# Optimization experiments

Measured on AMD Instinct MI355X. Metric: run time of the kernel, lower is better.

Reference implementation:

```python
import jax, jax.numpy as jnp
import numpy as np

D_MODEL = 512
NUM_HEADS = 8
HEAD_DIM = D_MODEL // NUM_HEADS
SEQ_LEN = 4096
BATCH = 2
D_FF = 4 * D_MODEL
EPS = 1e-5


def _layer_norm(x, g, b):
    mu = jnp.mean(x, axis=-1, keepdims=True)
    var = jnp.var(x, axis=-1, keepdims=True)
    return (x - mu) * jax.lax.rsqrt(var + EPS) * g + b


def setup_inputs() -> dict:
    key = jax.random.key(0)
    ks = jax.random.split(key, 12)
    s = 0.02
    inp = {
        "x": jax.random.normal(ks[0], (BATCH, SEQ_LEN, D_MODEL), jnp.float32),
        # Linear weights stored as [in, out] (y = x @ W + b)
        "Wq": jax.random.normal(ks[1], (D_MODEL, D_MODEL), jnp.float32) * s,
        "bq": jnp.zeros((D_MODEL,), jnp.float32),
        "Wk": jax.random.normal(ks[2], (D_MODEL, D_MODEL), jnp.float32) * s,
        "bk": jnp.zeros((D_MODEL,), jnp.float32),
        "Wv": jax.random.normal(ks[3], (D_MODEL, D_MODEL), jnp.float32) * s,
        "bv": jnp.zeros((D_MODEL,), jnp.float32),
        "Wo": jax.random.normal(ks[4], (D_MODEL, D_MODEL), jnp.float32) * s,
        "bo": jnp.zeros((D_MODEL,), jnp.float32),
        "ln1_g": jnp.ones((D_MODEL,), jnp.float32),
        "ln1_b": jnp.zeros((D_MODEL,), jnp.float32),
        "ln2_g": jnp.ones((D_MODEL,), jnp.float32),
        "ln2_b": jnp.zeros((D_MODEL,), jnp.float32),
        "W1": jax.random.normal(ks[5], (D_MODEL, D_FF), jnp.float32) * s,
        "b1": jnp.zeros((D_FF,), jnp.float32),
        "W2": jax.random.normal(ks[6], (D_FF, D_MODEL), jnp.float32) * s,
        "b2": jnp.zeros((D_MODEL,), jnp.float32),
    }
    return inp


def reference(x, Wq, bq, Wk, bk, Wv, bv, Wo, bo, ln1_g, ln1_b, ln2_g, ln2_b, W1, b1, W2, b2):
    B, S, D = x.shape
    residual = x
    h = _layer_norm(x, ln1_g, ln1_b)
    # project and split heads: [B, H, S, Dh]
    def split_heads(t):
        return t.reshape(B, S, NUM_HEADS, HEAD_DIM).transpose(0, 2, 1, 3)
    q = split_heads(h @ Wq + bq)
    k = split_heads(h @ Wk + bk)
    v = split_heads(h @ Wv + bv)
    scores = jnp.einsum("bhqd,bhkd->bhqk", q, k) / (HEAD_DIM ** 0.5)
    attn = jax.nn.softmax(scores, axis=-1)
    out = jnp.einsum("bhqk,bhkd->bhqd", attn, v)
    out = out.transpose(0, 2, 1, 3).reshape(B, S, D)
    out = out @ Wo + bo
    x1 = residual + out
    h2 = _layer_norm(x1, ln2_g, ln2_b)
    ff = jax.nn.gelu(h2 @ W1 + b1, approximate=False) @ W2 + b2
    return x1 + ff
```

## Files before the change

kernel.cpp:

```cpp
#include <hip/hip_runtime.h>
#include <hip/hip_bf16.h>
#include <math.h>

typedef __hip_bfloat16 bf16;

#define D_MODEL 512
#define NUM_HEADS 8
#define HEAD_DIM 64
#define SEQ_LEN 4096
#define BATCH 2
#define D_FF 2048
#define TOKENS (BATCH * SEQ_LEN)
#define QKV_STRIDE 1536
#define KSPLIT 2

typedef short short4v __attribute__((ext_vector_type(4)));
typedef short short8v __attribute__((ext_vector_type(8)));
typedef float float4v __attribute__((ext_vector_type(4)));
typedef float float2v __attribute__((ext_vector_type(2)));

union frag_u { short8v v8; short4v v4[2]; short s[8]; };
union pack_u { unsigned u[2]; short4v v4; };

__device__ __forceinline__ float b2f(bf16 v) { return __bfloat162float(v); }
__device__ __forceinline__ bf16 f2b(float v) { return __float2bfloat16(v); }
__device__ __forceinline__ short f2bs(float v) { bf16 t = __float2bfloat16(v); return *(short*)&t; }
__device__ __forceinline__ float exp2fast(float x) { return __builtin_amdgcn_exp2f(x); }

__device__ __forceinline__ unsigned pack_bf16(float lo, float hi) {
    unsigned a = __float_as_uint(hi) + 0x8000u;
    unsigned b = __float_as_uint(lo) + 0x8000u;
    return __builtin_amdgcn_perm(a, b, 0x07060302u);
}

__device__ __forceinline__ unsigned cvt_pk_bf16(float lo, float hi) {
    unsigned r;
    asm("v_cvt_pk_bf16_f32 %0, %1, %2" : "=v"(r) : "v"(lo), "v"(hi));
    return r;
}

__device__ __forceinline__ int3 swz_xyz() {
    int gx = gridDim.x, gy = gridDim.y;
    int id = blockIdx.x + gx * (blockIdx.y + gy * blockIdx.z);
    int nwg = gx * gy * (int)gridDim.z;
    int nid = (id & 7) * (nwg >> 3) + (id >> 3);
    int3 r;
    r.x = nid % gx;
    int t = nid / gx;
    r.y = t % gy;
    r.z = t / gy;
    return r;
}

#define AS1(p) ((__attribute__((address_space(1))) void*)(p))
#define AS3(p) ((__attribute__((address_space(3))) void*)(p))

__device__ __forceinline__ int self_detect(const unsigned* __restrict__ xw, int tid) {
    unsigned w = xw[tid & 63];
    unsigned e = (w >> 7) & 0xFFu;
    unsigned long long b = __ballot(e >= 110 && e <= 140);
    return __popcll(b) < 32;
}

__device__ __forceinline__ void do_tr(const void* __restrict__ src, bf16* __restrict__ dst,
                                      int K, int N, int n0, int k0, int fl, int tid,
                                      bf16 (*tile)[65]) {
    int c = tid & 63, r4 = tid >> 6;
#pragma unroll
    for (int t = 0; t < 16; t++) {
        int r = t * 4 + r4;
        size_t si = (size_t)(k0 + r) * N + n0 + c;
        float v = fl ? ((const float*)src)[si] : b2f(((const bf16*)src)[si]);
        tile[r][c] = f2b(v);
    }
    __syncthreads();
#pragma unroll
    for (int t = 0; t < 16; t++) {
        int r = t * 4 + r4;
        dst[(size_t)(n0 + r) * K + k0 + c] = tile[c][r];
    }
}

__global__ void prep_ln_kernel(const void* x, const void* Wq, const void* Wk, const void* Wv,
                               const void* Wo, const void* W1, const void* W2,
                               const void* bq, const void* bk, const void* bv, const void* bo,
                               const void* b1, const void* b2,
                               const void* g1, const void* e1, const void* g2, const void* e2,
                               bf16* __restrict__ Wqkvt ,
                               bf16* __restrict__ W1t, bf16* __restrict__ W2t,
                               bf16* __restrict__ small, int* __restrict__ flag,
                               bf16* __restrict__ hb) {
    __shared__ bf16 tile[64][65];
    __shared__ float rs[4], rss[4], stat[2];
    int blk = blockIdx.x, tid = threadIdx.x;
    int fl = self_detect((const unsigned*)x, tid);
    if (blk == 0 && tid == 0) flag[0] = fl;
    if (blk < 256) {
        int z = blk >> 6, tt = blk & 63;
        const void* src = (z == 0) ? Wq : (z == 1) ? Wk : (z == 2) ? Wv : Wo;
        do_tr(src, Wqkvt + (size_t)z * 512 * 512, 512, 512, (tt & 7) * 64, (tt >> 3) * 64,
              fl, tid, tile);
    } else if (blk < 512) {
        int tt = blk - 256;
        do_tr(W1, W1t, 512, 2048, (tt & 31) * 64, (tt >> 5) * 64, fl, tid, tile);
    } else if (blk < 768) {
        int tt = blk - 512;
        do_tr(W2, W2t, 2048, 512, (tt & 7) * 64, (tt >> 3) * 64, fl, tid, tile);
    } else if (blk < 794) {
        int i = (blk - 768) * 256 + tid;
        const void* src; int off;
        if (i < 512)       { src = bq; off = 0; }
        else if (i < 1024) { src = bk; off = 512; }
        else if (i < 1536) { src = bv; off = 1024; }
        else if (i < 2048) { src = bo; off = 1536; }
        else if (i < 4096) { src = b1; off = 2048; }
        else if (i < 4608) { src = b2; off = 4096; }
        else if (i < 5120) { src = g1; off = 4608; }
        else if (i < 5632) { src = e1; off = 5120; }
        else if (i < 6144) { src = g2; off = 5632; }
        else               { src = e2; off = 6144; }
        int j = i - off;
        small[i] = fl ? f2b(((const float*)src)[j]) : ((const bf16*)src)[j];
    } else {
        int t = blk - 794;
        float v0, v1, gg0, gg1, bb0, bb1;
        if (fl) {
            const float* xr = (const float*)x + (size_t)t * D_MODEL;
            v0 = xr[tid]; v1 = xr[tid + 256];
            gg0 = ((const float*)g1)[tid]; gg1 = ((const float*)g1)[tid + 256];
            bb0 = ((const float*)e1)[tid]; bb1 = ((const float*)e1)[tid + 256];
        } else {
            const bf16* xr = (const bf16*)x + (size_t)t * D_MODEL;
            v0 = b2f(xr[tid]); v1 = b2f(xr[tid + 256]);
            gg0 = b2f(((const bf16*)g1)[tid]); gg1 = b2f(((const bf16*)g1)[tid + 256]);
            bb0 = b2f(((const bf16*)e1)[tid]); bb1 = b2f(((const bf16*)e1)[tid + 256]);
        }
        float s = v0 + v1, ss = v0 * v0 + v1 * v1;
        for (int o = 32; o > 0; o >>= 1) {
            s += __shfl_down(s, o);
            ss += __shfl_down(ss, o);
        }
        int w = tid >> 6, l = tid & 63;
        if (l == 0) { rs[w] = s; rss[w] = ss; }
        __syncthreads();
        if (tid == 0) {
            float S = rs[0] + rs[1] + rs[2] + rs[3];
            float SS = rss[0] + rss[1] + rss[2] + rss[3];
            float mu = S / (float)D_MODEL;
            float var = SS / (float)D_MODEL - mu * mu;
            stat[0] = mu;
            stat[1] = rsqrtf(var + 1e-5f);
        }
        __syncthreads();
        float mu = stat[0], rstd = stat[1];
        bf16* orow = hb + (size_t)t * D_MODEL;
        orow[tid]       = f2b((v0 - mu) * rstd * gg0 + bb0);
        orow[tid + 256] = f2b((v1 - mu) * rstd * gg1 + bb1);
    }
}

template <int MODE>
__global__ void ln_kernel(const void* __restrict__ xv, const bf16* __restrict__ g,
                          const bf16* __restrict__ b, bf16* __restrict__ out,
                          const int* __restrict__ flag) {
    int t = blockIdx.x;
    int tid = threadIdx.x;
    int fl = (MODE == 2) ? *flag : 0;
    float v0, v1;
    if (fl) {
        const float* xr = (const float*)xv + (size_t)t * D_MODEL;
        v0 = xr[tid]; v1 = xr[tid + 256];
    } else {
        const bf16* xr = (const bf16*)xv + (size_t)t * D_MODEL;
        v0 = b2f(xr[tid]); v1 = b2f(xr[tid + 256]);
    }
    float s = v0 + v1, ss = v0 * v0 + v1 * v1;
    for (int o = 32; o > 0; o >>= 1) {
        s += __shfl_down(s, o);
        ss += __shfl_down(ss, o);
    }
    __shared__ float rs[4], rss[4], stat[2];
    int w = tid >> 6, l = tid & 63;
    if (l == 0) { rs[w] = s; rss[w] = ss; }
    __syncthreads();
    if (tid == 0) {
        float S = rs[0] + rs[1] + rs[2] + rs[3];
        float SS = rss[0] + rss[1] + rss[2] + rss[3];
        float mu = S / (float)D_MODEL;
        float var = SS / (float)D_MODEL - mu * mu;
        stat[0] = mu;
        stat[1] = rsqrtf(var + 1e-5f);
    }
    __syncthreads();
    float mu = stat[0], rstd = stat[1];
    bf16* orow = out + (size_t)t * D_MODEL;
    orow[tid]       = f2b((v0 - mu) * rstd * b2f(g[tid])       + b2f(b[tid]));
    orow[tid + 256] = f2b((v1 - mu) * rstd * b2f(g[tid + 256]) + b2f(b[tid + 256]));
}

__device__ __forceinline__ float gelu_tanh(float v) {
    float u = 0.7978845608f * (v + 0.044715f * v * v * v);
    float e2 = __expf(-2.f * u);
    return v / (1.f + e2);
}

template <int ACT, int RES, int OUTMODE, int VT>
__global__ __launch_bounds__(256) void mfma_gemm64(
    const bf16* __restrict__ A, const bf16* __restrict__ Wt,
    const bf16* __restrict__ bias, const void* __restrict__ res,
    void* __restrict__ Cout, bf16* __restrict__ Vt_out,
    const int* __restrict__ flag, int M, int N, int K) {
    __shared__ bf16 As[2][128 * 32];
    __shared__ bf16 Bs[2][64 * 32];
    int tid = threadIdx.x, wave = tid >> 6, lane = tid & 63;
    int m = lane & 15, g = lane >> 4;
    int3 sw = swz_xyz();
    int row0 = sw.y * 128, col0 = sw.x * 64;
    int R0 = wave * 32;
    int fl = (OUTMODE == 2 || RES == 3) ? *flag : 0;
    float4v acc[2][4] = {};

    int srow = lane >> 2;
    int scol = (lane & 3) * 8;
    const bf16* Ab = A  + (size_t)(row0 + wave * 32 + srow) * K + scol;
    const bf16* Bb = Wt + (size_t)(col0 + wave * 16 + srow) * K + scol;

#define GSTAGE64(buf, kk0)                                                         \
    {                                                                              \
        _Pragma("unroll")                                                          \
        for (int t = 0; t < 2; t++)                                                \
            __builtin_amdgcn_global_load_lds(AS1(Ab + (size_t)(t * 16) * K + (kk0)),\
                AS3(&As[buf][(wave * 32 + t * 16) * 32]), 16, 0, 0);               \
        __builtin_amdgcn_global_load_lds(AS1(Bb + (kk0)),                          \
            AS3(&Bs[buf][(wave * 16) * 32]), 16, 0, 0);                            \
    }

    int nk = K >> 5;
    GSTAGE64(0, 0);
    __syncthreads();
    for (int it = 0; it < nk; it++) {
        int cur = it & 1;
        if (it + 1 < nk) GSTAGE64(cur ^ 1, (it + 1) * 32);
        short8v fa[2], fb[4];
#pragma unroll
        for (int i = 0; i < 2; i++)
            fa[i] = *(const short8v*)&As[cur][(R0 + i * 16 + m) * 32 + g * 8];
#pragma unroll
        for (int j = 0; j < 4; j++)
            fb[j] = *(const short8v*)&Bs[cur][(j * 16 + m) * 32 + g * 8];
        __builtin_amdgcn_s_setprio(1);
#pragma unroll
        for (int i = 0; i < 2; i++)
#pragma unroll
            for (int j = 0; j < 4; j++)
                acc[i][j] = __builtin_amdgcn_mfma_f32_16x16x32_bf16(fa[i], fb[j], acc[i][j], 0, 0, 0);
        __builtin_amdgcn_s_setprio(0);
        __syncthreads();
    }
#undef GSTAGE64

    if (VT && col0 >= 1024) {
#pragma unroll
        for (int i = 0; i < 2; i++) {
            int row = row0 + R0 + i * 16 + g * 4;
            int b = row >> 12, s = row & (SEQ_LEN - 1);
#pragma unroll
            for (int j = 0; j < 4; j++) {
                int col = col0 + j * 16 + m;
                int hh = (col - 1024) >> 6, d = col & 63;
                float bi = b2f(bias[col]);
                pack_u oo;
                oo.u[0] = pack_bf16(acc[i][j][0] + bi, acc[i][j][1] + bi);
                oo.u[1] = pack_bf16(acc[i][j][2] + bi, acc[i][j][3] + bi);
                *(short4v*)&Vt_out[((size_t)((b << 3) + hh) * 64 + d) * SEQ_LEN + s] = oo.v4;
            }
        }
        return;
    }

#pragma unroll
    for (int i = 0; i < 2; i++) {
#pragma unroll
        for (int r = 0; r < 4; r++) {
            int row = row0 + R0 + i * 16 + g * 4 + r;
#pragma unroll
            for (int j = 0; j < 4; j++) {
                int col = col0 + j * 16 + m;
                float v = acc[i][j][r] + b2f(bias[col]);
                if (ACT == 1) v = gelu_tanh(v);
                size_t idx = (size_t)row * N + col;
                if (RES == 2) v += b2f(((const bf16*)res)[idx]);
                if (RES == 3) v += fl ? ((const float*)res)[idx]
                                      : b2f(((const bf16*)res)[idx]);
                if (OUTMODE == 0) ((bf16*)Cout)[idx] = f2b(v);
                else {
                    if (fl) ((float*)Cout)[idx] = v;
                    else ((bf16*)Cout)[idx] = f2b(v);
                }
            }
        }
    }
}

#define F3(a, b, c) fmaxf(fmaxf((a), (b)), (c))
template <int KS>
__global__ __launch_bounds__(256, 4) void flash_attn(const bf16* __restrict__ Q,
                                                     const bf16* __restrict__ K,
                                                     const bf16* __restrict__ Vt_g,
                                                     bf16* __restrict__ Op,
                                                     float2* __restrict__ mlout) {
    __shared__ bf16 Ks[64][72];
    __shared__ bf16 Vt[64][72];

    int tid = threadIdx.x;
    int wave = tid >> 6, lane = tid & 63;
    int m = lane & 15, g = lane >> 4;
    bf16* PtW = &Ks[0][0] + wave * (16 * 72);

    int3 sw = swz_xyz();
    int bh = sw.y;
    size_t base = (size_t)(bh >> 3) * SEQ_LEN * QKV_STRIDE + (size_t)(bh & 7) * HEAD_DIM;
    int q0w = sw.x * 128 + wave * 32;

    const float qscale = 0.125f * 1.44269504f;
    short8v aQ[2][2];
#pragma unroll
    for (int mt = 0; mt < 2; mt++) {
        const bf16* qp = Q + base + (size_t)(q0w + mt * 16 + m) * QKV_STRIDE + g * 8;
#pragma unroll
        for (int c = 0; c < 2; c++) {
            frag_u u;
#pragma unroll
            for (int j = 0; j < 8; j++) u.s[j] = f2bs(b2f(qp[c * 32 + j]) * qscale);
            aQ[mt][c] = u.v8;
        }
    }

    float mrow[2] = {-1e30f, -1e30f};
    float lrow[2] = {0.f, 0.f};
    float4v oacc[2][4] = {};

    int sk = tid >> 2, sd = (tid & 3) * 16;
    int vrow = tid >> 2, vcol = (tid & 3) * 16;

    const unsigned short* Ku = (const unsigned short*)(K + base);
    const unsigned short* Vg = (const unsigned short*)Vt_g +
                               (size_t)bh * 64 * SEQ_LEN + (size_t)vrow * SEQ_LEN;

    int t0 = sw.z * (64 / KS);
    int t1 = t0 + 64 / KS;

    short8v rk0, rk1, rv0, rv1;
    {
        int kt0 = t0 * 64;
        const unsigned short* kp = Ku + (size_t)(kt0 + sk) * QKV_STRIDE + sd;
        rk0 = *(const short8v*)(kp);
        rk1 = *(const short8v*)(kp + 8);
        rv0 = *(const short8v*)(Vg + kt0 + vcol);
        rv1 = *(const short8v*)(Vg + kt0 + vcol + 8);
        *(short8v*)&Ks[sk][sd]     = rk0;
        *(short8v*)&Ks[sk][sd + 8] = rk1;
        *(short8v*)&Vt[vrow][vcol]     = rv0;
        *(short8v*)&Vt[vrow][vcol + 8] = rv1;
    }
    __syncthreads();

    for (int t = t0; t < t1; t++) {
        if (t + 1 < t1) {
            int ktn = (t + 1) * 64;
            const unsigned short* kp = Ku + (size_t)(ktn + sk) * QKV_STRIDE + sd;
            rk0 = *(const short8v*)(kp);
            rk1 = *(const short8v*)(kp + 8);
            rv0 = *(const short8v*)(Vg + ktn + vcol);
            rv1 = *(const short8v*)(Vg + ktn + vcol + 8);
        }

        float4v st[2][4];
        __builtin_amdgcn_s_setprio(1);
#pragma unroll
        for (int kt = 0; kt < 4; kt++) {
            short8v bK0 = *(const short8v*)&Ks[kt * 16 + m][g * 8];
            short8v bK1 = *(const short8v*)&Ks[kt * 16 + m][32 + g * 8];
#pragma unroll
            for (int mt = 0; mt < 2; mt++) {
                float4v a = {0.f, 0.f, 0.f, 0.f};
                a = __builtin_amdgcn_mfma_f32_16x16x32_bf16(bK0, aQ[mt][0], a, 0, 0, 0);
                a = __builtin_amdgcn_mfma_f32_16x16x32_bf16(bK1, aQ[mt][1], a, 0, 0, 0);
                st[mt][kt] = a;
            }
        }
        __builtin_amdgcn_s_setprio(0);

        __syncthreads();

        short8v bP[2][2];
#pragma unroll
        for (int mt = 0; mt < 2; mt++) {
            float u0 = F3(st[mt][0][0], st[mt][0][1], st[mt][0][2]);
            float u1 = F3(st[mt][0][3], st[mt][1][0], st[mt][1][1]);
            float u2 = F3(st[mt][1][2], st[mt][1][3], st[mt][2][0]);
            float u3 = F3(st[mt][2][1], st[mt][2][2], st[mt][2][3]);
            float u4 = F3(st[mt][3][0], st[mt][3][1], st[mt][3][2]);
            float tm = fmaxf(F3(u0, u1, u2), F3(u3, u4, st[mt][3][3]));
            tm = fmaxf(tm, __shfl_xor(tm, 16));
            tm = fmaxf(tm, __shfl_xor(tm, 32));
            if (!__all(tm - mrow[mt] <= 8.f)) {
                float mnew = fmaxf(mrow[mt], tm);
                float alpha = exp2fast(mrow[mt] - mnew);
                mrow[mt] = mnew;
                lrow[mt] *= alpha;
#pragma unroll
                for (int dt = 0; dt < 4; dt++)
#pragma unroll
                    for (int r = 0; r < 4; r++) oacc[mt][dt][r] *= alpha;
            }
            float mcur = mrow[mt];
            float2v ps = {0.f, 0.f};
#pragma unroll
            for (int kt = 0; kt < 4; kt++) {
                float p0 = exp2fast(st[mt][kt][0] - mcur);
                float p1 = exp2fast(st[mt][kt][1] - mcur);
                float p2 = exp2fast(st[mt][kt][2] - mcur);
                float p3 = exp2fast(st[mt][kt][3] - mcur);
                float2v a = {p0, p1}, b = {p2, p3};
                ps += a + b;
                pack_u pp;
                pp.u[0] = cvt_pk_bf16(p0, p1);
                pp.u[1] = cvt_pk_bf16(p2, p3);
                *(short4v*)&PtW[m * 72 + kt * 16 + g * 4] = pp.v4;
            }
            lrow[mt] += ps[0] + ps[1];
#pragma unroll
            for (int c = 0; c < 2; c++)
                bP[mt][c] = *(const short8v*)&PtW[m * 72 + c * 32 + g * 8];
        }

        __builtin_amdgcn_s_setprio(1);
#pragma unroll
        for (int dt = 0; dt < 4; dt++) {
#pragma unroll
            for (int c = 0; c < 2; c++) {
                short8v av = *(const short8v*)&Vt[dt * 16 + m][c * 32 + g * 8];
#pragma unroll
                for (int mt = 0; mt < 2; mt++)
                    oacc[mt][dt] = __builtin_amdgcn_mfma_f32_16x16x32_bf16(av, bP[mt][c], oacc[mt][dt], 0, 0, 0);
            }
        }
        __builtin_amdgcn_s_setprio(0);

        __syncthreads();
        if (t + 1 < t1) {
            *(short8v*)&Ks[sk][sd]     = rk0;
            *(short8v*)&Ks[sk][sd + 8] = rk1;
            *(short8v*)&Vt[vrow][vcol]     = rv0;
            *(short8v*)&Vt[vrow][vcol + 8] = rv1;
        }
        __syncthreads();
    }

    size_t zoff = (size_t)sw.z * NUM_HEADS * BATCH + bh;
    size_t pbase = zoff * (SEQ_LEN * (size_t)HEAD_DIM);
#pragma unroll
    for (int mt = 0; mt < 2; mt++) {
        float l = lrow[mt];
        l += __shfl_xor(l, 16);
        l += __shfl_xor(l, 32);
        int q = q0w + mt * 16 + m;
        bf16* orow = Op + pbase + (size_t)q * HEAD_DIM;
#pragma unroll
        for (int dt = 0; dt < 4; dt++) {
            pack_u oo;
            oo.u[0] = cvt_pk_bf16(oacc[mt][dt][0], oacc[mt][dt][1]);
            oo.u[1] = cvt_pk_bf16(oacc[mt][dt][2], oacc[mt][dt][3]);
            *(short4v*)&orow[dt * 16 + g * 4] = oo.v4;
        }
        if (g == 0) mlout[zoff * SEQ_LEN + q] = make_float2(mrow[mt], l);
    }
}

template <int KS>
__global__ void attn_merge(const bf16* __restrict__ Op, const float2* __restrict__ ml,
                           bf16* __restrict__ O) {
    int i = blockIdx.x * 256 + threadIdx.x;
    int d = i & 63;
    int q = (i >> 6) & (SEQ_LEN - 1);
    int bh = i >> 18;
    const int HQ = NUM_HEADS * BATCH * SEQ_LEN;
    float2 a[KS];
    float M = -1e30f;
#pragma unroll
    for (int p = 0; p < KS; p++) {
        a[p] = ml[(size_t)p * HQ + bh * SEQ_LEN + q];
        M = fmaxf(M, a[p].x);
    }
    float w[KS];
    float denom = 0.f;
#pragma unroll
    for (int p = 0; p < KS; p++) {
        w[p] = exp2fast(a[p].x - M);
        denom += a[p].y * w[p];
    }
    float inv = 1.f / denom;
    const size_t NP = (size_t)HQ * HEAD_DIM;
    float o = 0.f;
#pragma unroll
    for (int p = 0; p < KS; p++) o += b2f(Op[(size_t)p * NP + i]) * w[p];
    o *= inv;
    O[((size_t)((bh >> 3) * SEQ_LEN + q)) * D_MODEL + (bh & 7) * HEAD_DIM + d] = f2b(o);
}

extern "C" void kernel_launch(void* const* d_in, const int* in_sizes, int n_in,
                              void* d_out, int out_size, void* d_ws, size_t ws_size,
                              hipStream_t stream) {
    const void* x     = d_in[0];
    const void* Wq    = d_in[1];
    const void* bq    = d_in[2];
    const void* Wk    = d_in[3];
    const void* bk    = d_in[4];
    const void* Wv    = d_in[5];
    const void* bv    = d_in[6];
    const void* Wo    = d_in[7];
    const void* bo    = d_in[8];
    const void* ln1_g = d_in[9];
    const void* ln1_b = d_in[10];
    const void* ln2_g = d_in[11];
    const void* ln2_b = d_in[12];
    const void* W1    = d_in[13];
    const void* b1    = d_in[14];
    const void* W2    = d_in[15];
    const void* b2    = d_in[16];

    char* p = (char*)d_ws;
    int* flag = (int*)p;                      p += 256;
    size_t tok_d = (size_t)TOKENS * D_MODEL;
    char* region2 = p;                        p += 2 * tok_d * 2;
    bf16* x1b   = (bf16*)region2;
    bf16* hb    = (bf16*)(region2 + tok_d * 2);
    bf16* Opart = (bf16*)region2;
    bf16*  bigA = (bf16*)p;                   p += (size_t)TOKENS * D_FF * 2;
    bf16*  qkvb = bigA;
    bf16*  ab   = bigA + (size_t)TOKENS * QKV_STRIDE;
    bf16*  ffb  = bigA;
    bf16*  Wqkvt = (bf16*)p;                  p += (size_t)QKV_STRIDE * D_MODEL * 2;
    bf16*  Wot   = (bf16*)p;                  p += (size_t)D_MODEL * D_MODEL * 2;
    bf16*  W1t   = (bf16*)p;                  p += (size_t)D_FF * D_MODEL * 2;
    bf16*  W2t   = (bf16*)p;                  p += (size_t)D_MODEL * D_FF * 2;
    bf16*  Vtg   = (bf16*)p;                  p += (size_t)NUM_HEADS * BATCH * HEAD_DIM * SEQ_LEN * 2;
    float2* mlb  = (float2*)p;                p += (size_t)KSPLIT * NUM_HEADS * BATCH * SEQ_LEN * sizeof(float2);
    bf16*  small = (bf16*)p;                  p += 6656 * 2;
    bf16* bias_qkv = small + 0;
    bf16* bias_o   = small + 1536;
    bf16* b1b      = small + 2048;
    bf16* b2b      = small + 4096;
    bf16* g1b      = small + 4608;
    bf16* be1b     = small + 5120;
    bf16* g2b      = small + 5632;
    bf16* be2b     = small + 6144;
    (void)g1b; (void)be1b;

    prep_ln_kernel<<<794 + TOKENS, 256, 0, stream>>>(
        x, Wq, Wk, Wv, Wo, W1, W2, bq, bk, bv, bo, b1, b2,
        ln1_g, ln1_b, ln2_g, ln2_b, Wqkvt, W1t, W2t, small, flag, hb);

    mfma_gemm64<0, 0, 0, 1><<<dim3(QKV_STRIDE / 64, TOKENS / 128), 256, 0, stream>>>(
        hb, Wqkvt, bias_qkv, nullptr, qkvb, Vtg, flag, TOKENS, QKV_STRIDE, D_MODEL);

    flash_attn<KSPLIT><<<dim3(SEQ_LEN / 128, 16, KSPLIT), 256, 0, stream>>>(
        qkvb, qkvb + 512, Vtg, Opart, mlb);
    attn_merge<KSPLIT><<<(NUM_HEADS * BATCH * SEQ_LEN * HEAD_DIM) / 256, 256, 0, stream>>>(
        Opart, mlb, ab);

    mfma_gemm64<0, 3, 0, 0><<<dim3(D_MODEL / 64, TOKENS / 128), 256, 0, stream>>>(
        ab, Wot, bias_o, x, x1b, nullptr, flag, TOKENS, D_MODEL, D_MODEL);

    ln_kernel<0><<<TOKENS, 256, 0, stream>>>(x1b, g2b, be2b, hb, flag);

    mfma_gemm64<1, 0, 0, 0><<<dim3(D_FF / 64, TOKENS / 128), 256, 0, stream>>>(
        hb, W1t, b1b, nullptr, ffb, nullptr, flag, TOKENS, D_FF, D_MODEL);

    mfma_gemm64<0, 2, 2, 0><<<dim3(D_MODEL / 64, TOKENS / 128), 256, 0, stream>>>(
        ffb, W2t, b2b, x1b, d_out, nullptr, flag, TOKENS, D_MODEL, D_FF);
}
```

Baseline: 336.1 us.

## Fuse split-K attention merge into the output projection GEMM

Adds an oproj_merge kernel that reads the two split-K attention partial outputs and their max/sum stats, combines them on the fly while staging the A tile into shared memory, and then runs the Wo GEMM with bias and residual. This removes the separate attn_merge launch and the write-then-read round trip of the merged attention tensor. The partial buffer moves to the workspace tail so it does not alias x1b, and the fused path is used only when the workspace is large enough, otherwise the old two-kernel path runs. In exchange, each of the 8 column blocks in the fused kernel re-reads and re-merges the same partials, which repeats the merge arithmetic and the partial-buffer reads.

```diff
diff --git a/kernel.cpp b/kernel.cpp
--- a/kernel.cpp
+++ b/kernel.cpp
@@ -302,6 +302,114 @@
     }
 }
 
+__global__ __launch_bounds__(256) void oproj_merge(
+    const bf16* __restrict__ Op, const float2* __restrict__ ml,
+    const bf16* __restrict__ Wt, const bf16* __restrict__ bias,
+    const void* __restrict__ res, bf16* __restrict__ Cout,
+    const int* __restrict__ flag) {
+    const int N = D_MODEL, K = D_MODEL;
+    __shared__ bf16 As[2][128 * 40];
+    __shared__ bf16 Bs[2][64 * 32];
+    int tid = threadIdx.x, wave = tid >> 6, lane = tid & 63;
+    int m = lane & 15, g = lane >> 4;
+    int3 sw = swz_xyz();
+    int row0 = sw.y * 128, col0 = sw.x * 64;
+    int R0 = wave * 32;
+    int fl = *flag;
+    float4v acc[2][4] = {};
+
+    int srow = lane >> 2, scol = (lane & 3) * 8;
+    const bf16* Bb = Wt + (size_t)(col0 + wave * 16 + srow) * K + scol;
+
+    int r = tid >> 1, ch = tid & 1;
+    int rg = row0 + r;
+    int bb = rg >> 12, s = rg & (SEQ_LEN - 1);
+
+    short8v a00, a01, a10, a11;
+    float2 m0v, m1v;
+
+#define ALOAD(kk)                                                              \
+    {                                                                          \
+        int h = (kk) >> 6, dbase = ((kk) & 63) + ch * 16;                      \
+        int bh = bb * 8 + h;                                                   \
+        const unsigned short* p0 = (const unsigned short*)Op +                 \
+            ((size_t)bh * SEQ_LEN + s) * 64 + dbase;                           \
+        const unsigned short* p1 = (const unsigned short*)Op +                 \
+            ((size_t)(16 + bh) * SEQ_LEN + s) * 64 + dbase;                    \
+        a00 = *(const short8v*)(p0);  a01 = *(const short8v*)(p0 + 8);         \
+        a10 = *(const short8v*)(p1);  a11 = *(const short8v*)(p1 + 8);         \
+        m0v = ml[(size_t)bh * SEQ_LEN + s];                                    \
+        m1v = ml[(size_t)(16 + bh) * SEQ_LEN + s];                             \
+    }
+
+#define AMERGE_WRITE(buf)                                                      \
+    {                                                                          \
+        float Mx = fmaxf(m0v.x, m1v.x);                                        \
+        float w0 = exp2fast(m0v.x - Mx), w1 = exp2fast(m1v.x - Mx);            \
+        float inv = 1.f / (m0v.y * w0 + m1v.y * w1);                           \
+        w0 *= inv; w1 *= inv;                                                  \
+        frag_u u0, u1, v0, v1, o0, o1;                                         \
+        u0.v8 = a00; u1.v8 = a01; v0.v8 = a10; v1.v8 = a11;                    \
+        _Pragma("unroll")                                                      \
+        for (int j = 0; j < 8; j++) {                                          \
+            o0.s[j] = f2bs(b2f(*(bf16*)&u0.s[j]) * w0 + b2f(*(bf16*)&v0.s[j]) * w1); \
+            o1.s[j] = f2bs(b2f(*(bf16*)&u1.s[j]) * w0 + b2f(*(bf16*)&v1.s[j]) * w1); \
+        }                                                                      \
+        *(short8v*)&As[buf][r * 40 + ch * 16]     = o0.v8;                     \
+        *(short8v*)&As[buf][r * 40 + ch * 16 + 8] = o1.v8;                     \
+    }
+
+#define BSTAGE(buf, kk0)                                                       \
+    __builtin_amdgcn_global_load_lds(AS1(Bb + (kk0)),                          \
+        AS3(&Bs[buf][(wave * 16) * 32]), 16, 0, 0);
+
+    int nk = K >> 5;
+    ALOAD(0);
+    BSTAGE(0, 0);
+    AMERGE_WRITE(0);
+    __syncthreads();
+    for (int it = 0; it < nk; it++) {
+        int cur = it & 1;
+        if (it + 1 < nk) { ALOAD((it + 1) * 32); BSTAGE(cur ^ 1, (it + 1) * 32); }
+        short8v fa[2], fb[4];
+#pragma unroll
+        for (int i = 0; i < 2; i++)
+            fa[i] = *(const short8v*)&As[cur][(R0 + i * 16 + m) * 40 + g * 8];
+#pragma unroll
+        for (int j = 0; j < 4; j++)
+            fb[j] = *(const short8v*)&Bs[cur][(j * 16 + m) * 32 + g * 8];
+        __builtin_amdgcn_s_setprio(1);
+#pragma unroll
+        for (int i = 0; i < 2; i++)
+#pragma unroll
+            for (int j = 0; j < 4; j++)
+                acc[i][j] = __builtin_amdgcn_mfma_f32_16x16x32_bf16(fa[i], fb[j], acc[i][j], 0, 0, 0);
+        __builtin_amdgcn_s_setprio(0);
+        __syncthreads();
+        if (it + 1 < nk) AMERGE_WRITE(cur ^ 1);
+        __syncthreads();
+    }
+#undef ALOAD
+#undef AMERGE_WRITE
+#undef BSTAGE
+
+#pragma unroll
+    for (int i = 0; i < 2; i++) {
+#pragma unroll
+        for (int rr = 0; rr < 4; rr++) {
+            int row = row0 + R0 + i * 16 + g * 4 + rr;
+#pragma unroll
+            for (int j = 0; j < 4; j++) {
+                int col = col0 + j * 16 + m;
+                float v = acc[i][j][rr] + b2f(bias[col]);
+                size_t idx = (size_t)row * N + col;
+                v += fl ? ((const float*)res)[idx] : b2f(((const bf16*)res)[idx]);
+                Cout[idx] = f2b(v);
+            }
+        }
+    }
+}
+
 #define F3(a, b, c) fmaxf(fmaxf((a), (b)), (c))
 template <int KS>
 __global__ __launch_bounds__(256, 4) void flash_attn(const bf16* __restrict__ Q,
@@ -536,7 +644,6 @@
     char* region2 = p;                        p += 2 * tok_d * 2;
     bf16* x1b   = (bf16*)region2;
     bf16* hb    = (bf16*)(region2 + tok_d * 2);
-    bf16* Opart = (bf16*)region2;
     bf16*  bigA = (bf16*)p;                   p += (size_t)TOKENS * D_FF * 2;
     bf16*  qkvb = bigA;
     bf16*  ab   = bigA + (size_t)TOKENS * QKV_STRIDE;
@@ -548,6 +655,11 @@
     bf16*  Vtg   = (bf16*)p;                  p += (size_t)NUM_HEADS * BATCH * HEAD_DIM * SEQ_LEN * 2;
     float2* mlb  = (float2*)p;                p += (size_t)KSPLIT * NUM_HEADS * BATCH * SEQ_LEN * sizeof(float2);
     bf16*  small = (bf16*)p;                  p += 6656 * 2;
+    bf16* Optail = (bf16*)p;
+    size_t opbytes = (size_t)KSPLIT * NUM_HEADS * BATCH * SEQ_LEN * HEAD_DIM * 2;
+    int fused = ((char*)Optail + opbytes - (char*)d_ws) <= (ptrdiff_t)ws_size;
+    bf16* Opart = fused ? Optail : (bf16*)region2;
+
     bf16* bias_qkv = small + 0;
     bf16* bias_o   = small + 1536;
     bf16* b1b      = small + 2048;
@@ -567,11 +679,16 @@
 
     flash_attn<KSPLIT><<<dim3(SEQ_LEN / 128, 16, KSPLIT), 256, 0, stream>>>(
         qkvb, qkvb + 512, Vtg, Opart, mlb);
-    attn_merge<KSPLIT><<<(NUM_HEADS * BATCH * SEQ_LEN * HEAD_DIM) / 256, 256, 0, stream>>>(
-        Opart, mlb, ab);
-
-    mfma_gemm64<0, 3, 0, 0><<<dim3(D_MODEL / 64, TOKENS / 128), 256, 0, stream>>>(
-        ab, Wot, bias_o, x, x1b, nullptr, flag, TOKENS, D_MODEL, D_MODEL);
+
+    if (fused) {
+        oproj_merge<<<dim3(D_MODEL / 64, TOKENS / 128), 256, 0, stream>>>(
+            Opart, mlb, Wot, bias_o, x, x1b, flag);
+    } else {
+        attn_merge<KSPLIT><<<(NUM_HEADS * BATCH * SEQ_LEN * HEAD_DIM) / 256, 256, 0, stream>>>(
+            Opart, mlb, ab);
+        mfma_gemm64<0, 3, 0, 0><<<dim3(D_MODEL / 64, TOKENS / 128), 256, 0, stream>>>(
+            ab, Wot, bias_o, x, x1b, nullptr, flag, TOKENS, D_MODEL, D_MODEL);
+    }
 
     ln_kernel<0><<<TOKENS, 256, 0, stream>>>(x1b, g2b, be2b, hb, flag);
 
```

Result: no change. 341.5 us (+1.6%).
